# Kernel tuning notes

Hardware: AMD Instinct MI355X
Metric: run time of the kernel (lower is better)

Reference implementation:

```python
import jax, jax.numpy as jnp
import numpy as np

DAYS = 288
DIMS = 40
B, T, N, D = 16, 12, 325, 64
HEAD_DIM = D // 8  # geo(4)+sem(2)+t(2) heads


def setup_inputs() -> dict:
    key = jax.random.key(0)
    ks = jax.random.split(key, 20)
    f = lambda k, s: jax.random.normal(k, s, dtype=jnp.float32)
    inp = {
        "x": f(ks[0], (B, T, N, D)),
        "ind": jax.random.randint(ks[1], (B,), 0, DAYS),
        "x_patterns": jnp.zeros((B, T, N, 1), jnp.float32),
        "pattern_keys": jnp.zeros((B, T, N, 1), jnp.float32),
        "geo_mask": jax.random.randint(ks[2], (N, N), 0, 2).astype(bool),
        # dynamic-graph node embeddings
        "p1": f(ks[3], (DAYS, DIMS)),
        "p2": f(ks[4], (N, DIMS)),
        "p3": f(ks[5], (N, DIMS)),
        "pk": f(ks[6], (DIMS, DIMS, DIMS)),
        # reshape1: Linear(D -> 32)
        "W_r1": f(ks[7], (32, D)) * 0.05, "b_r1": jnp.zeros((32,), jnp.float32),
        # gcn mlp: 1x1 conv, in=(2*1+1)*32=96, out=32
        "W_gcn": f(ks[8], (32, 96)) * 0.05, "b_gcn": jnp.zeros((32,), jnp.float32),
        # reshape2: Linear(32 -> D)
        "W_r2": f(ks[9], (D, 32)) * 0.05, "b_r2": jnp.zeros((D,), jnp.float32),
        # temporal q/k/v 1x1 convs: D -> D*t_ratio = 16, no bias
        "Wtq": f(ks[10], (16, D)) * 0.05,
        "Wtk": f(ks[11], (16, D)) * 0.05,
        "Wtv": f(ks[12], (16, D)) * 0.05,
        # geo q/k/v 1x1 convs: D -> D*geo_ratio = 32, no bias
        "Wgq": f(ks[13], (32, D)) * 0.05,
        "Wgk": f(ks[14], (32, D)) * 0.05,
        "Wgv": f(ks[15], (32, D)) * 0.05,
        # proj: Linear(3D/4 = 48 -> D)
        "W_proj": f(ks[16], (D, 48)) * 0.05, "b_proj": jnp.zeros((D,), jnp.float32),
    }
    return inp


def reference(x, ind, x_patterns, pattern_keys, geo_mask,
              p1, p2, p3, pk,
              W_r1, b_r1, W_gcn, b_gcn, W_r2, b_r2,
              Wtq, Wtk, Wtv, Wgq, Wgk, Wgv, W_proj, b_proj):
    Bx, Tx, Nx, Dx = x.shape
    scale = HEAD_DIM ** -0.5

    # --- dgconstruct: dynamic adjacency [B, N, N]
    te = p1[ind % DAYS]                                  # (B, dims)
    adp = jnp.einsum('ai,ijk->ajk', te, pk)              # (B, dims, dims)
    adp = jnp.einsum('bj,ajk->abk', p2, adp)             # (B, N, dims)
    adp = jnp.einsum('ck,abk->abc', p3, adp)             # (B, N, N)
    adp = jax.nn.softmax(jax.nn.relu(adp), axis=2)

    # --- reshape1 + order-2 GCN + reshape2 (eval mode: dropout off)
    h = jnp.einsum('btnd,cd->bcnt', x, W_r1) + b_r1[None, :, None, None]  # (B,32,N,T)
    x1 = jnp.einsum('ncvl,nwv->ncwl', h, adp)
    x2 = jnp.einsum('ncvl,nwv->ncwl', x1, adp)
    hcat = jnp.concatenate([h, x1, x2], axis=1)          # (B,96,N,T)
    g = jnp.einsum('bcnt,oc->bont', hcat, W_gcn) + b_gcn[None, :, None, None]  # (B,32,N,T)
    xg = jnp.einsum('bont,do->btnd', g, W_r2) + b_r2     # (B,T,N,D)

    # --- temporal attention (2 heads over T, per node)
    t_q = jnp.einsum('btnd,od->bnto', xg, Wtq).reshape(Bx, Nx, Tx, 2, HEAD_DIM).transpose(0, 1, 3, 2, 4)
    t_k = jnp.einsum('btnd,od->bnto', xg, Wtk).reshape(Bx, Nx, Tx, 2, HEAD_DIM).transpose(0, 1, 3, 2, 4)
    t_v = jnp.einsum('btnd,od->bnto', xg, Wtv).reshape(Bx, Nx, Tx, 2, HEAD_DIM).transpose(0, 1, 3, 2, 4)
    t_attn = jax.nn.softmax(jnp.einsum('bnhqd,bnhkd->bnhqk', t_q, t_k) * scale, axis=-1)
    t_x = jnp.einsum('bnhqk,bnhkd->bnhqd', t_attn, t_v)  # (B,N,2,T,hd)
    t_x = t_x.transpose(0, 1, 3, 2, 4).reshape(Bx, Nx, Tx, 2 * HEAD_DIM).transpose(0, 2, 1, 3)  # (B,T,N,16)

    # --- geo attention (4 heads over N, per timestep) with bool mask
    g_q = jnp.einsum('btnd,od->btno', xg, Wgq).reshape(Bx, Tx, Nx, 4, HEAD_DIM).transpose(0, 1, 3, 2, 4)
    g_k = jnp.einsum('btnd,od->btno', xg, Wgk).reshape(Bx, Tx, Nx, 4, HEAD_DIM).transpose(0, 1, 3, 2, 4)
    g_v = jnp.einsum('btnd,od->btno', xg, Wgv).reshape(Bx, Tx, Nx, 4, HEAD_DIM).transpose(0, 1, 3, 2, 4)
    g_attn = jnp.einsum('bthqd,bthkd->bthqk', g_q, g_k) * scale  # (B,T,4,N,N)
    g_attn = jnp.where(geo_mask, -jnp.inf, g_attn)
    g_attn = jax.nn.softmax(g_attn, axis=-1)
    geo_x = jnp.einsum('bthqk,bthkd->bthqd', g_attn, g_v)        # (B,T,4,N,hd)
    geo_x = geo_x.transpose(0, 1, 3, 2, 4).reshape(Bx, Tx, Nx, 4 * HEAD_DIM)  # (B,T,N,32)

    out = jnp.concatenate([t_x, geo_x], axis=-1) @ W_proj.T + b_proj  # (B,T,N,D)
    return out
```

## Files before the change

### kernel.cpp

```cpp
#include <hip/hip_runtime.h>
#include <hip/hip_bf16.h>
#include <math.h>

#define B_ 16
#define T_ 12
#define N_ 325
#define DIMS_ 40
#define DAYS_ 288
#define MW 12
#define NQP 336
#define VP 352

typedef __attribute__((ext_vector_type(8))) short bf16x8;
typedef __attribute__((ext_vector_type(4))) float f32x4;

__device__ __forceinline__ unsigned short cvt1(float f){
  unsigned w;
  asm("v_cvt_pk_bf16_f32 %0, %1, %2" : "=v"(w) : "v"(f), "v"(f));
  return (unsigned short)w;
}
__device__ __forceinline__ unsigned cvt2(float a, float b){
  unsigned w;
  asm("v_cvt_pk_bf16_f32 %0, %1, %2" : "=v"(w) : "v"(a), "v"(b));
  return w;
}
__device__ __forceinline__ bf16x8 u2b(uint4 u){ return __builtin_bit_cast(bf16x8, u); }

__global__ void setup_k(const float* __restrict__ p1, const float* __restrict__ pk,
                        const int* __restrict__ ind, float* __restrict__ A1,
                        const unsigned char* __restrict__ raw, unsigned* __restrict__ bm,
                        const float* __restrict__ p3, float* __restrict__ p3t,
                        const float* W_gcn, const float* b_gcn, const float* W_r2, const float* b_r2,
                        const float* Wtq, const float* Wtk, const float* Wtv,
                        const float* Wgq, const float* Wgk, const float* Wgv,
                        const float* W_proj, const float* W_r1,
                        float* bc, unsigned short* Wcb, unsigned short* Wallb,
                        unsigned short* Wpb, unsigned short* Wr1b){
  int tid = threadIdx.x;
  if (blockIdx.x < 16){
    int b = blockIdx.x;
    __shared__ float te[DIMS_];
    int day = ind[b] % DAYS_; if (day < 0) day += DAYS_;
    for (int i = tid; i < DIMS_; i += blockDim.x) te[i] = p1[day*DIMS_ + i];
    __syncthreads();
    for (int jk = tid; jk < DIMS_*DIMS_; jk += blockDim.x){
      float acc = 0.f;
      for (int i = 0; i < DIMS_; ++i) acc += te[i] * pk[i*DIMS_*DIMS_ + jk];
      A1[b*DIMS_*DIMS_ + jk] = acc;
    }
  } else if (blockIdx.x < 32){
    __shared__ int f1, f3, fo;
    if (tid == 0){ f1 = 0; f3 = 0; fo = 0; }
    __syncthreads();
    for (int i = tid; i < 4096; i += 256){
      unsigned char v = raw[i];
      int m4 = i & 3;
      if (v == 0x3F && m4 == 1) atomicOr(&f1, 1);
      if (v == 0x3F && m4 == 3) atomicOr(&f3, 1);
      if (v != 0 && m4 != 0)    atomicOr(&fo, 1);
    }
    __syncthreads();
    int mode = f1 ? 2 : (f3 ? 3 : (fo ? 0 : 1));
    int idx = (blockIdx.x - 16) * 256 + tid;
    if (idx >= NQP * MW) return;
    int q = idx / MW, w = idx % MW;
    if (q >= N_) { bm[idx] = 0xFFFFFFFFu; return; }
    unsigned bits = 0;
    for (int j = 0; j < 32; ++j){
      int k = w*32 + j;
      int v;
      if (k >= N_) v = 1;
      else {
        size_t i = (size_t)q*N_ + k;
        if (mode == 0)      v = raw[i] != 0;
        else if (mode == 1) v = ((const int*)raw)[i] != 0;
        else if (mode == 2) { unsigned short u = ((const unsigned short*)raw)[i]; v = (u & 0x7FFF) != 0; }
        else                { float f = ((const float*)raw)[i]; v = (f != 0.f); }
      }
      bits |= (unsigned)v << j;
    }
    bm[idx] = bits;
  } else if (blockIdx.x == 32){
    for (int idx = tid; idx < DIMS_*N_; idx += 256){
      int k = idx / N_, c = idx % N_;
      p3t[idx] = p3[c*DIMS_ + k];
    }
  } else if (blockIdx.x == 33){
    __shared__ float WcS[64*96];
    for (int idx = tid; idx < 64*96; idx += 256){
      int d = idx / 96, c = idx % 96;
      float acc = 0.f;
      for (int o = 0; o < 32; ++o) acc += W_r2[d*32 + o] * W_gcn[o*96 + c];
      WcS[idx] = acc;
    }
    for (int d = tid; d < 64; d += 256){
      float acc = b_r2[d];
      for (int o = 0; o < 32; ++o) acc += W_r2[d*32 + o] * b_gcn[o];
      bc[d] = acc;
    }
    __syncthreads();
    for (int idx = tid; idx < 3*4*64*8; idx += 256){
      int jj = idx & 7, rest = idx >> 3;
      int d = rest % 64, gk = rest / 64;
      int g = gk & 3, kc = gk >> 2;
      Wcb[idx] = cvt1(WcS[d*96 + kc*32 + g*8 + jj]);
    }
  } else if (blockIdx.x == 34){
    for (int idx = tid; idx < 2*4*144*8; idx += 256){
      int jj = idx & 7, rest = idx >> 3;
      int j = rest % 144, gk = rest / 144;
      int g = gk & 3, kc = gk >> 2;
      int dd = kc*32 + g*8 + jj;
      const float* src; int rsrc;
      if      (j < 16) { src = Wtq; rsrc = j; }
      else if (j < 32) { src = Wtk; rsrc = j - 16; }
      else if (j < 48) { src = Wtv; rsrc = j - 32; }
      else if (j < 80) { src = Wgq; rsrc = j - 48; }
      else if (j < 112){ src = Wgk; rsrc = j - 80; }
      else             { src = Wgv; rsrc = j - 112; }
      Wallb[idx] = cvt1(src[rsrc*64 + dd]);
    }
  } else if (blockIdx.x == 35){
    for (int idx = tid; idx < 2*4*64*8; idx += 256){
      int jj = idx & 7, rest = idx >> 3;
      int d = rest % 64, gk = rest / 64;
      int g = gk & 3, kc = gk >> 2;
      int k = kc*32 + g*8 + jj;
      Wpb[idx] = (k < 48) ? cvt1(W_proj[d*48 + k]) : (unsigned short)0;
    }
  } else {
    for (int idx = tid; idx < 2*4*32*8; idx += 256){
      int jj = idx & 7, rest = idx >> 3;
      int c = rest % 32, gk = rest / 32;
      int g = gk & 3, kc = gk >> 2;
      Wr1b[idx] = cvt1(W_r1[c*64 + kc*32 + g*8 + jj]);
    }
  }
}

__global__ void dg_adp(const float* __restrict__ p2, const float* __restrict__ p3t,
                       const float* __restrict__ A1, unsigned short* __restrict__ adp_bf){
  int bid = blockIdx.x; int b = bid / N_; int n = bid % N_;
  __shared__ float p2r[DIMS_], t2[DIMS_], sbuf[N_], red[128];
  int tid = threadIdx.x;
  if (tid < DIMS_) p2r[tid] = p2[n*DIMS_ + tid];
  __syncthreads();
  if (tid < DIMS_){
    float acc = 0.f;
    const float* a1 = A1 + b*DIMS_*DIMS_;
    for (int j = 0; j < DIMS_; ++j) acc += p2r[j] * a1[j*DIMS_ + tid];
    t2[tid] = acc;
  }
  __syncthreads();
  float lm = -INFINITY;
  for (int c = tid; c < N_; c += 128){
    float acc = 0.f;
    for (int k = 0; k < DIMS_; ++k) acc += p3t[k*N_ + c] * t2[k];
    acc = fmaxf(acc, 0.f);
    sbuf[c] = acc; lm = fmaxf(lm, acc);
  }
  red[tid] = lm; __syncthreads();
  for (int off = 64; off; off >>= 1){ if (tid < off) red[tid] = fmaxf(red[tid], red[tid+off]); __syncthreads(); }
  float m = red[0]; __syncthreads();
  float ls = 0.f;
  for (int c = tid; c < N_; c += 128){ float e = __expf(sbuf[c] - m); sbuf[c] = e; ls += e; }
  red[tid] = ls; __syncthreads();
  for (int off = 64; off; off >>= 1){ if (tid < off) red[tid] += red[tid+off]; __syncthreads(); }
  float inv = 1.f / red[0];
  unsigned short* outp = adp_bf + ((size_t)b*N_ + n) * VP;
  for (int c = tid; c < VP; c += 128)
    outp[c] = (c < N_) ? cvt1(sbuf[c] * inv) : (unsigned short)0;
}

__global__ __launch_bounds__(256) void hproj_mfma(const float* __restrict__ x,
                                                  const unsigned short* __restrict__ Wr1b,
                                                  const float* __restrict__ b_r1,
                                                  unsigned short* __restrict__ ht,
                                                  unsigned short* __restrict__ hn){
  int tid = threadIdx.x, wv = tid >> 6, ln = tid & 63;
  int bt = blockIdx.x / 6;
  int nt = (blockIdx.x % 6)*4 + wv;
  if (nt >= 21) return;
  int g = ln >> 4, r = ln & 15;
  int n0 = nt*16;
  int nc = min(n0 + r, N_-1);
  int b = bt / T_, t = bt % T_;
  const float* xrow = x + ((size_t)bt*N_ + nc)*64;
  float4 xa = *(const float4*)&xrow[g*8];
  float4 xb = *(const float4*)&xrow[g*8 + 4];
  uint4 u0 = { cvt2(xa.x,xa.y), cvt2(xa.z,xa.w), cvt2(xb.x,xb.y), cvt2(xb.z,xb.w) };
  bf16x8 bv0 = u2b(u0);
  float4 xc = *(const float4*)&xrow[32 + g*8];
  float4 xd = *(const float4*)&xrow[32 + g*8 + 4];
  uint4 u1 = { cvt2(xc.x,xc.y), cvt2(xc.z,xc.w), cvt2(xd.x,xd.y), cvt2(xd.z,xd.w) };
  bf16x8 bv1 = u2b(u1);
  int n = n0 + r;
  #pragma unroll
  for (int ct = 0; ct < 2; ++ct){
    f32x4 acc = {0.f,0.f,0.f,0.f};
    bf16x8 a0 = *(const bf16x8*)&Wr1b[((0*4+g)*32 + ct*16 + r)*8];
    bf16x8 a1 = *(const bf16x8*)&Wr1b[((1*4+g)*32 + ct*16 + r)*8];
    acc = __builtin_amdgcn_mfma_f32_16x16x32_bf16(a0, bv0, acc, 0,0,0);
    acc = __builtin_amdgcn_mfma_f32_16x16x32_bf16(a1, bv1, acc, 0,0,0);
    if (n < N_){
      float v0 = acc[0] + b_r1[ct*16 + g*4 + 0];
      float v1 = acc[1] + b_r1[ct*16 + g*4 + 1];
      float v2 = acc[2] + b_r1[ct*16 + g*4 + 2];
      float v3 = acc[3] + b_r1[ct*16 + g*4 + 3];
      int c0 = ct*16 + g*4;
      ht[((size_t)b*384 + t*32 + c0+0)*VP + n] = cvt1(v0);
      ht[((size_t)b*384 + t*32 + c0+1)*VP + n] = cvt1(v1);
      ht[((size_t)b*384 + t*32 + c0+2)*VP + n] = cvt1(v2);
      ht[((size_t)b*384 + t*32 + c0+3)*VP + n] = cvt1(v3);
      uint2 hp = { cvt2(v0, v1), cvt2(v2, v3) };
      *(uint2*)&hn[((size_t)b*N_ + n)*384 + t*32 + c0] = hp;
    }
  }
}

__global__ __launch_bounds__(256) void gcn_mfma(const unsigned short* __restrict__ adp_bf,
                                                const unsigned short* __restrict__ in_t,
                                                unsigned short* __restrict__ out_t,
                                                unsigned short* __restrict__ out_n){
  int bi = blockIdx.x;
  int b = bi / 36, rest = bi % 36;
  int wt = rest / 6, ctb = rest % 6;
  int tid = threadIdx.x, wv = tid >> 6, ln = tid & 63, g = ln >> 4, r = ln & 15;
  int w0 = wt*64 + wv*16;
  int ct0 = ctb*64;
  int wr = min(w0 + r, N_-1);
  const unsigned short* arow  = adp_bf + ((size_t)b*N_ + wr)*VP;
  const unsigned short* bbase = in_t  + ((size_t)b*384 + ct0)*VP;
  f32x4 acc0={0.f,0.f,0.f,0.f}, acc1=acc0, acc2=acc0, acc3=acc0;
  #pragma unroll
  for (int ks = 0; ks < 11; ++ks){
    int ko = ks*32 + g*8;
    bf16x8 a  = *(const bf16x8*)&arow[ko];
    bf16x8 b0 = *(const bf16x8*)&bbase[(size_t)( 0 + r)*VP + ko];
    bf16x8 b1 = *(const bf16x8*)&bbase[(size_t)(16 + r)*VP + ko];
    bf16x8 b2 = *(const bf16x8*)&bbase[(size_t)(32 + r)*VP + ko];
    bf16x8 b3 = *(const bf16x8*)&bbase[(size_t)(48 + r)*VP + ko];
    acc0 = __builtin_amdgcn_mfma_f32_16x16x32_bf16(a, b0, acc0, 0,0,0);
    acc1 = __builtin_amdgcn_mfma_f32_16x16x32_bf16(a, b1, acc1, 0,0,0);
    acc2 = __builtin_amdgcn_mfma_f32_16x16x32_bf16(a, b2, acc2, 0,0,0);
    acc3 = __builtin_amdgcn_mfma_f32_16x16x32_bf16(a, b3, acc3, 0,0,0);
  }
  f32x4 av[4] = {acc0, acc1, acc2, acc3};
  if (out_t && w0 + 15 < VP){
    #pragma unroll
    for (int dt = 0; dt < 4; ++dt){
      int ct = ct0 + dt*16 + r;
      uint2 pk2 = { cvt2(av[dt][0], av[dt][1]), cvt2(av[dt][2], av[dt][3]) };
      *(uint2*)&out_t[((size_t)b*384 + ct)*VP + w0 + g*4] = pk2;
    }
  }
  #pragma unroll
  for (int dt = 0; dt < 4; ++dt){
    int ct = ct0 + dt*16 + r;
    #pragma unroll
    for (int rg = 0; rg < 4; ++rg){
      int w = w0 + g*4 + rg;
      if (w < N_) out_n[((size_t)b*N_ + w)*384 + ct] = cvt1(av[dt][rg]);
    }
  }
}

__global__ __launch_bounds__(256) void xg_k(const unsigned short* __restrict__ hn,
                                            const unsigned short* __restrict__ x1n,
                                            const unsigned short* __restrict__ x2n,
                                            const unsigned short* __restrict__ Wcb,
                                            const float* __restrict__ bc,
                                            unsigned short* __restrict__ xg_bf){
  int tid = threadIdx.x, wv = tid >> 6, ln = tid & 63;
  int p = blockIdx.x*4 + wv;
  int b = p / N_, n = p % N_;
  int g = ln >> 4, r = ln & 15;
  int rr = min(r, 11);
  size_t base = ((size_t)b*N_ + n)*384;
  bf16x8 a0 = *(const bf16x8*)&hn [base + rr*32 + g*8];
  bf16x8 a1 = *(const bf16x8*)&x1n[base + rr*32 + g*8];
  bf16x8 a2 = *(const bf16x8*)&x2n[base + rr*32 + g*8];
  #pragma unroll
  for (int dt = 0; dt < 4; ++dt){
    f32x4 acc = {0.f,0.f,0.f,0.f};
    bf16x8 b0 = *(const bf16x8*)&Wcb[((0*4+g)*64 + dt*16 + r)*8];
    bf16x8 b1 = *(const bf16x8*)&Wcb[((1*4+g)*64 + dt*16 + r)*8];
    bf16x8 b2 = *(const bf16x8*)&Wcb[((2*4+g)*64 + dt*16 + r)*8];
    acc = __builtin_amdgcn_mfma_f32_16x16x32_bf16(a0, b0, acc, 0,0,0);
    acc = __builtin_amdgcn_mfma_f32_16x16x32_bf16(a1, b1, acc, 0,0,0);
    acc = __builtin_amdgcn_mfma_f32_16x16x32_bf16(a2, b2, acc, 0,0,0);
    float bias = bc[dt*16 + r];
    if (g < 3){
      #pragma unroll
      for (int rg = 0; rg < 4; ++rg){
        int t = g*4 + rg;
        xg_bf[(((size_t)b*T_ + t)*N_ + n)*64 + dt*16 + r] = cvt1(acc[rg] + bias);
      }
    }
  }
}

__global__ __launch_bounds__(256) void qkv_k(const unsigned short* __restrict__ xg_bf,
                                             const unsigned short* __restrict__ Wallb,
                                             float* __restrict__ qkv48,
                                             unsigned short* __restrict__ Qg,
                                             unsigned short* __restrict__ Kg,
                                             unsigned short* __restrict__ Vg){
  int tid = threadIdx.x, wv = tid >> 6, ln = tid & 63;
  int bt = blockIdx.x / 6;
  int nt = (blockIdx.x % 6)*4 + wv;
  if (nt >= 21) return;
  int g = ln >> 4, r = ln & 15;
  int n0 = nt*16;
  int nc = min(n0 + r, N_-1);
  const unsigned short* arow = xg_bf + ((size_t)bt*N_ + nc)*64;
  bf16x8 a0 = *(const bf16x8*)&arow[g*8];
  bf16x8 a1 = *(const bf16x8*)&arow[32 + g*8];
  const float kscale = 0.35355339059327373f * 1.4426950408889634f;
  int hh = r >> 3, dd = r & 7;
  #pragma unroll
  for (int jt = 0; jt < 9; ++jt){
    f32x4 acc = {0.f,0.f,0.f,0.f};
    bf16x8 b0 = *(const bf16x8*)&Wallb[((0*4+g)*144 + jt*16 + r)*8];
    bf16x8 b1 = *(const bf16x8*)&Wallb[((1*4+g)*144 + jt*16 + r)*8];
    acc = __builtin_amdgcn_mfma_f32_16x16x32_bf16(a0, b0, acc, 0,0,0);
    acc = __builtin_amdgcn_mfma_f32_16x16x32_bf16(a1, b1, acc, 0,0,0);
    #pragma unroll
    for (int rg = 0; rg < 4; ++rg){
      int n = n0 + g*4 + rg;
      if (n >= N_) continue;
      float v = acc[rg];
      if (jt < 3){
        qkv48[((size_t)bt*N_ + n)*48 + jt*16 + r] = v;
      } else if (jt < 5){
        int h = (jt-3)*2 + hh;
        Qg[(((size_t)bt*4 + h)*N_ + n)*8 + dd] = cvt1(v);
      } else if (jt < 7){
        int h = (jt-5)*2 + hh;
        Kg[(((size_t)bt*4 + h)*352 + n)*8 + dd] = cvt1(v * kscale);
      } else {
        int h = (jt-7)*2 + hh;
        int m = n & 31, ks = n >> 5;
        int p32 = (((m & 15) >> 2) << 3) | (m & 3) | ((m & 16) >> 2);
        Vg[(((size_t)bt*4 + h)*11 + ks)*512 + dd*32 + p32] = cvt1(v);
      }
    }
  }
}

__global__ __launch_bounds__(256) void attn_fused(const float* __restrict__ qkv48,
                                                  const unsigned short* __restrict__ Qg,
                                                  const unsigned short* __restrict__ Kg,
                                                  const unsigned short* __restrict__ Vg,
                                                  const unsigned* __restrict__ bm,
                                                  float* __restrict__ att){
  __shared__ __align__(16) char smem[17408];
  int bid = blockIdx.x;
  int tid = threadIdx.x, wv = tid >> 6, ln = tid & 63;
  if (bid < 4032){
    unsigned short* Kb = (unsigned short*)smem;
    unsigned short* Vt = (unsigned short*)(smem + 5632);
    int bt = (bid & 7)*24 + (bid >> 3)/21;
    int blkin = (bid >> 3) % 21;
    int unit = blkin*4 + wv;
    int h = unit / 21, tile = unit % 21;
    int g = ln >> 4, r = ln & 15, g4 = g*4;
    bool gzero = (g == 0);
    const bf16x8 z8 = {0,0,0,0,0,0,0,0};
    size_t hb = (size_t)bt*4 + h;
    int qb = tile*16;
    int qc = min(qb + r, N_-1);
    const uint4* bmp = (const uint4*)(bm + (size_t)(qb + r)*MW);
    uint4 m0 = bmp[0], m1 = bmp[1], m2 = bmp[2];
    unsigned bmw[11] = {m0.x,m0.y,m0.z,m0.w, m1.x,m1.y,m1.z,m1.w, m2.x,m2.y,m2.z};
    bf16x8 aq = z8;
    if (gzero) aq = *(const bf16x8*)&Qg[(hb*N_ + qc)*8];
    const unsigned short* Kh = Kg + hb*352*8;
    const unsigned short* Vh = Vg + hb*11*512;
    float ssum = 0.f;
    f32x4 acc = {0.f,0.f,0.f,0.f};
    #pragma unroll
    for (int ks = 0; ks < 11; ++ks){
      bf16x8 akA = z8, akB = z8;
      if (gzero){
        akA = *(const bf16x8*)&Kh[(ks*32 + r)*8];
        akB = *(const bf16x8*)&Kh[(ks*32 + 16 + r)*8];
      }
      f32x4 dA = {0.f,0.f,0.f,0.f}, dB = {0.f,0.f,0.f,0.f};
      dA = __builtin_amdgcn_mfma_f32_16x16x32_bf16(akA, aq, dA, 0,0,0);
      dB = __builtin_amdgcn_mfma_f32_16x16x32_bf16(akB, aq, dB, 0,0,0);
      unsigned wm = bmw[ks];
      unsigned bA = (wm >> g4) & 0xFu;
      unsigned bB = (wm >> (g4 + 16)) & 0xFu;
      float pA[4], pB[4];
      #pragma unroll
      for (int rg = 0; rg < 4; ++rg){
        float eA = exp2f(dA[rg]);
        float eB = exp2f(dB[rg]);
        eA = (bA & (1u << rg)) ? 0.f : eA;
        eB = (bB & (1u << rg)) ? 0.f : eB;
        ssum += eA; ssum += eB;
        pA[rg] = eA; pB[rg] = eB;
      }
      uint4 pw = { cvt2(pA[0],pA[1]), cvt2(pA[2],pA[3]),
                   cvt2(pB[0],pB[1]), cvt2(pB[2],pB[3]) };
      bf16x8 avv = *(const bf16x8*)&Vh[ks*512 + r*32 + g*8];
      acc = __builtin_amdgcn_mfma_f32_16x16x32_bf16(avv, u2b(pw), acc, 0,0,0);
    }
    ssum += __shfl_xor(ssum, 16);
    ssum += __shfl_xor(ssum, 32);
    float inv = (ssum > 0.f) ? __builtin_amdgcn_rcpf(ssum) : 0.f;
    int qq = qb + r;
    if (g < 2 && qq < N_){
      float4 o = make_float4(acc[0]*inv, acc[1]*inv, acc[2]*inv, acc[3]*inv);
      *(float4*)(att + ((size_t)bt*N_ + qq)*48 + 16 + h*8 + g4) = o;
    }
    (void)Kb; (void)Vt;
  } else {
    int p = (bid - 4032)*4 + wv;
    int b = p / N_, n = p % N_;
    float* qs = (float*)smem + (size_t)wv*576;
    float* ss = (float*)(smem + 9216) + (size_t)wv*288;
    for (int idx = ln; idx < T_*48; idx += 64){
      int t = idx / 48, j = idx % 48;
      qs[idx] = qkv48[(((size_t)b*T_ + t)*N_ + n)*48 + j];
    }
    const float scale = 0.35355339059327373f;
    for (int idx = ln; idx < 2*T_*T_; idx += 64){
      int hh = idx / 144, r2 = (idx / T_) % T_, c = idx % T_;
      float acc = 0.f;
      for (int d = 0; d < 8; ++d) acc += qs[r2*48 + hh*8 + d] * qs[c*48 + 16 + hh*8 + d];
      ss[idx] = acc * scale;
    }
    if (ln < 2*T_){
      int hh = ln / T_, r2 = ln % T_;
      float* row = ss + hh*144 + r2*T_;
      float m = -INFINITY; for (int k = 0; k < T_; ++k) m = fmaxf(m, row[k]);
      float s = 0.f; for (int k = 0; k < T_; ++k){ float e = __expf(row[k] - m); row[k] = e; s += e; }
      float inv = 1.f / s; for (int k = 0; k < T_; ++k) row[k] *= inv;
    }
    for (int idx = ln; idx < T_*16; idx += 64){
      int t = idx / 16, o = idx % 16; int hh = o / 8, d = o % 8;
      float acc = 0.f;
      const float* row = ss + hh*144 + t*T_;
      for (int k = 0; k < T_; ++k) acc += row[k] * qs[k*48 + 32 + hh*8 + d];
      att[(((size_t)b*T_ + t)*N_ + n)*48 + o] = acc;
    }
  }
}

__global__ __launch_bounds__(256) void proj_k(const float* __restrict__ att,
                                              const unsigned short* __restrict__ Wpb,
                                              const float* __restrict__ b_proj,
                                              float* __restrict__ out){
  int tid = threadIdx.x, wv = tid >> 6, ln = tid & 63;
  int g = ln >> 4, r = ln & 15;
  long r0 = ((long)blockIdx.x*4 + wv)*16;
  const float* arow = att + (r0 + r)*48;
  float4 qa = *(const float4*)&arow[g*8];
  float4 qb = *(const float4*)&arow[g*8 + 4];
  uint4 u0 = { cvt2(qa.x,qa.y), cvt2(qa.z,qa.w), cvt2(qb.x,qb.y), cvt2(qb.z,qb.w) };
  bf16x8 a0 = u2b(u0);
  bf16x8 a1 = {0,0,0,0,0,0,0,0};
  if (g < 2){
    float4 qc = *(const float4*)&arow[32 + g*8];
    float4 qd = *(const float4*)&arow[36 + g*8];
    uint4 u1 = { cvt2(qc.x,qc.y), cvt2(qc.z,qc.w), cvt2(qd.x,qd.y), cvt2(qd.z,qd.w) };
    a1 = u2b(u1);
  }
  #pragma unroll
  for (int dt = 0; dt < 4; ++dt){
    f32x4 acc = {0.f,0.f,0.f,0.f};
    bf16x8 b0 = *(const bf16x8*)&Wpb[((0*4+g)*64 + dt*16 + r)*8];
    bf16x8 b1 = *(const bf16x8*)&Wpb[((1*4+g)*64 + dt*16 + r)*8];
    acc = __builtin_amdgcn_mfma_f32_16x16x32_bf16(a0, b0, acc, 0,0,0);
    acc = __builtin_amdgcn_mfma_f32_16x16x32_bf16(a1, b1, acc, 0,0,0);
    float bias = b_proj[dt*16 + r];
    #pragma unroll
    for (int rg = 0; rg < 4; ++rg)
      out[(r0 + g*4 + rg)*64 + dt*16 + r] = acc[rg] + bias;
  }
}

extern "C" void kernel_launch(void* const* d_in, const int* in_sizes, int n_in,
                              void* d_out, int out_size, void* d_ws, size_t ws_size,
                              hipStream_t stream){
  const float* x      = (const float*)d_in[0];
  const int*   ind    = (const int*)  d_in[1];
  const unsigned char* gmask_raw = (const unsigned char*)d_in[4];
  const float* p1     = (const float*)d_in[5];
  const float* p2     = (const float*)d_in[6];
  const float* p3     = (const float*)d_in[7];
  const float* pk     = (const float*)d_in[8];
  const float* W_r1   = (const float*)d_in[9];
  const float* b_r1   = (const float*)d_in[10];
  const float* W_gcn  = (const float*)d_in[11];
  const float* b_gcn  = (const float*)d_in[12];
  const float* W_r2   = (const float*)d_in[13];
  const float* b_r2   = (const float*)d_in[14];
  const float* Wtq    = (const float*)d_in[15];
  const float* Wtk    = (const float*)d_in[16];
  const float* Wtv    = (const float*)d_in[17];
  const float* Wgq    = (const float*)d_in[18];
  const float* Wgk    = (const float*)d_in[19];
  const float* Wgv    = (const float*)d_in[20];
  const float* W_proj = (const float*)d_in[21];
  const float* b_proj = (const float*)d_in[22];
  float* out = (float*)d_out;

  float* ws = (float*)d_ws;
  float* A1    = ws; ws += B_*DIMS_*DIMS_;
  float* bc    = ws; ws += 64;
  float* p3t   = ws; ws += DIMS_*N_;
  float* qkv48 = ws; ws += (size_t)B_*T_*N_*48;
  float* att   = ws; ws += (size_t)B_*T_*N_*48;
  unsigned* bm = (unsigned*)ws; ws += NQP*MW;
  unsigned short* us = (unsigned short*)ws;
  unsigned short* adp_bf = us; us += (size_t)B_*N_*VP;
  unsigned short* ht     = us; us += (size_t)B_*384*VP;
  unsigned short* x1t    = us; us += (size_t)B_*384*VP;
  unsigned short* hn     = us; us += (size_t)B_*N_*384;
  unsigned short* x1n    = us; us += (size_t)B_*N_*384;
  unsigned short* x2n    = us; us += (size_t)B_*N_*384;
  unsigned short* xg_bf  = us; us += (size_t)B_*T_*N_*64;
  unsigned short* Qg     = us; us += (size_t)192*4*N_*8;
  unsigned short* Kg     = us; us += (size_t)192*4*352*8;
  unsigned short* Vg     = us; us += (size_t)192*4*11*512;
  unsigned short* Wcb    = us; us += 3*4*64*8;
  unsigned short* Wallb  = us; us += 2*4*144*8;
  unsigned short* Wpb    = us; us += 2*4*64*8;
  unsigned short* Wr1b   = us; us += 2*4*32*8;

  setup_k     <<<37,        256, 0, stream>>>(p1, pk, ind, A1, gmask_raw, bm, p3, p3t,
                                              W_gcn, b_gcn, W_r2, b_r2,
                                              Wtq, Wtk, Wtv, Wgq, Wgk, Wgv,
                                              W_proj, W_r1, bc, Wcb, Wallb, Wpb, Wr1b);
  dg_adp      <<<B_*N_,     128, 0, stream>>>(p2, p3t, A1, adp_bf);
  hproj_mfma  <<<192*6,     256, 0, stream>>>(x, Wr1b, b_r1, ht, hn);
  gcn_mfma    <<<B_*36,     256, 0, stream>>>(adp_bf, ht,  x1t, x1n);
  gcn_mfma    <<<B_*36,     256, 0, stream>>>(adp_bf, x1t, (unsigned short*)nullptr, x2n);
  xg_k        <<<(B_*N_)/4, 256, 0, stream>>>(hn, x1n, x2n, Wcb, bc, xg_bf);
  qkv_k       <<<192*6,     256, 0, stream>>>(xg_bf, Wallb, qkv48, Qg, Kg, Vg);
  attn_fused  <<<4032+1300, 256, 0, stream>>>(qkv48, Qg, Kg, Vg, bm, att);
  proj_k      <<<(B_*T_*N_/16)/4, 256, 0, stream>>>(att, Wpb, b_proj, out);
}
```

Baseline: 154.3 us.

## Merge adjacency softmax and input projection into one heterogeneous launch

```diff
diff --git a/kernel.cpp b/kernel.cpp
--- a/kernel.cpp
+++ b/kernel.cpp
@@ -33,9 +33,9 @@
                         const float* W_gcn, const float* b_gcn, const float* W_r2, const float* b_r2,
                         const float* Wtq, const float* Wtk, const float* Wtv,
                         const float* Wgq, const float* Wgk, const float* Wgv,
-                        const float* W_proj, const float* W_r1,
+                        const float* W_proj,
                         float* bc, unsigned short* Wcb, unsigned short* Wallb,
-                        unsigned short* Wpb, unsigned short* Wr1b){
+                        unsigned short* Wpb){
   int tid = threadIdx.x;
   if (blockIdx.x < 16){
     int b = blockIdx.x;
@@ -120,7 +120,7 @@
       else             { src = Wgv; rsrc = j - 112; }
       Wallb[idx] = cvt1(src[rsrc*64 + dd]);
     }
-  } else if (blockIdx.x == 35){
+  } else {
     for (int idx = tid; idx < 2*4*64*8; idx += 256){
       int jj = idx & 7, rest = idx >> 3;
       int d = rest % 64, gk = rest / 64;
@@ -128,92 +128,106 @@
       int k = kc*32 + g*8 + jj;
       Wpb[idx] = (k < 48) ? cvt1(W_proj[d*48 + k]) : (unsigned short)0;
     }
+  }
+}
+
+__global__ __launch_bounds__(256) void mid_k(const float* __restrict__ x,
+                                             const float* __restrict__ W_r1,
+                                             const float* __restrict__ b_r1,
+                                             unsigned short* __restrict__ ht,
+                                             unsigned short* __restrict__ hn,
+                                             const float* __restrict__ p2,
+                                             const float* __restrict__ p3t,
+                                             const float* __restrict__ A1,
+                                             unsigned short* __restrict__ adp_bf){
+  __shared__ float t2s[4][DIMS_];
+  int tid = threadIdx.x, wv = tid >> 6, ln = tid & 63;
+  int bid = blockIdx.x;
+  if (bid < 1152){
+    int bt = bid / 6;
+    int nt = (bid % 6)*4 + wv;
+    if (nt >= 21) return;
+    int g = ln >> 4, r = ln & 15;
+    int n0 = nt*16;
+    int nc = min(n0 + r, N_-1);
+    int b = bt / T_, t = bt % T_;
+    const float* xrow = x + ((size_t)bt*N_ + nc)*64;
+    float4 xa = *(const float4*)&xrow[g*8];
+    float4 xb = *(const float4*)&xrow[g*8 + 4];
+    uint4 u0 = { cvt2(xa.x,xa.y), cvt2(xa.z,xa.w), cvt2(xb.x,xb.y), cvt2(xb.z,xb.w) };
+    bf16x8 bv0 = u2b(u0);
+    float4 xc = *(const float4*)&xrow[32 + g*8];
+    float4 xd = *(const float4*)&xrow[32 + g*8 + 4];
+    uint4 u1 = { cvt2(xc.x,xc.y), cvt2(xc.z,xc.w), cvt2(xd.x,xd.y), cvt2(xd.z,xd.w) };
+    bf16x8 bv1 = u2b(u1);
+    int n = n0 + r;
+    #pragma unroll
+    for (int ct = 0; ct < 2; ++ct){
+      const float* wrow = W_r1 + (ct*16 + r)*64;
+      float4 wa = *(const float4*)&wrow[g*8];
+      float4 wb = *(const float4*)&wrow[g*8 + 4];
+      uint4 ua = { cvt2(wa.x,wa.y), cvt2(wa.z,wa.w), cvt2(wb.x,wb.y), cvt2(wb.z,wb.w) };
+      bf16x8 a0 = u2b(ua);
+      float4 wc = *(const float4*)&wrow[32 + g*8];
+      float4 wd = *(const float4*)&wrow[32 + g*8 + 4];
+      uint4 ub = { cvt2(wc.x,wc.y), cvt2(wc.z,wc.w), cvt2(wd.x,wd.y), cvt2(wd.z,wd.w) };
+      bf16x8 a1 = u2b(ub);
+      f32x4 acc = {0.f,0.f,0.f,0.f};
+      acc = __builtin_amdgcn_mfma_f32_16x16x32_bf16(a0, bv0, acc, 0,0,0);
+      acc = __builtin_amdgcn_mfma_f32_16x16x32_bf16(a1, bv1, acc, 0,0,0);
+      if (n < N_){
+        float v0 = acc[0] + b_r1[ct*16 + g*4 + 0];
+        float v1 = acc[1] + b_r1[ct*16 + g*4 + 1];
+        float v2 = acc[2] + b_r1[ct*16 + g*4 + 2];
+        float v3 = acc[3] + b_r1[ct*16 + g*4 + 3];
+        int c0 = ct*16 + g*4;
+        ht[((size_t)b*384 + t*32 + c0+0)*VP + n] = cvt1(v0);
+        ht[((size_t)b*384 + t*32 + c0+1)*VP + n] = cvt1(v1);
+        ht[((size_t)b*384 + t*32 + c0+2)*VP + n] = cvt1(v2);
+        ht[((size_t)b*384 + t*32 + c0+3)*VP + n] = cvt1(v3);
+        uint2 hp = { cvt2(v0, v1), cvt2(v2, v3) };
+        *(uint2*)&hn[((size_t)b*N_ + n)*384 + t*32 + c0] = hp;
+      }
+    }
   } else {
-    for (int idx = tid; idx < 2*4*32*8; idx += 256){
-      int jj = idx & 7, rest = idx >> 3;
-      int c = rest % 32, gk = rest / 32;
-      int g = gk & 3, kc = gk >> 2;
-      Wr1b[idx] = cvt1(W_r1[c*64 + kc*32 + g*8 + jj]);
-    }
-  }
-}
-
-__global__ void dg_adp(const float* __restrict__ p2, const float* __restrict__ p3t,
-                       const float* __restrict__ A1, unsigned short* __restrict__ adp_bf){
-  int bid = blockIdx.x; int b = bid / N_; int n = bid % N_;
-  __shared__ float p2r[DIMS_], t2[DIMS_], sbuf[N_], red[128];
-  int tid = threadIdx.x;
-  if (tid < DIMS_) p2r[tid] = p2[n*DIMS_ + tid];
-  __syncthreads();
-  if (tid < DIMS_){
-    float acc = 0.f;
+    int p = (bid - 1152)*4 + wv;
+    int b = p / N_, n = p % N_;
     const float* a1 = A1 + b*DIMS_*DIMS_;
-    for (int j = 0; j < DIMS_; ++j) acc += p2r[j] * a1[j*DIMS_ + tid];
-    t2[tid] = acc;
-  }
-  __syncthreads();
-  float lm = -INFINITY;
-  for (int c = tid; c < N_; c += 128){
-    float acc = 0.f;
-    for (int k = 0; k < DIMS_; ++k) acc += p3t[k*N_ + c] * t2[k];
-    acc = fmaxf(acc, 0.f);
-    sbuf[c] = acc; lm = fmaxf(lm, acc);
-  }
-  red[tid] = lm; __syncthreads();
-  for (int off = 64; off; off >>= 1){ if (tid < off) red[tid] = fmaxf(red[tid], red[tid+off]); __syncthreads(); }
-  float m = red[0]; __syncthreads();
-  float ls = 0.f;
-  for (int c = tid; c < N_; c += 128){ float e = __expf(sbuf[c] - m); sbuf[c] = e; ls += e; }
-  red[tid] = ls; __syncthreads();
-  for (int off = 64; off; off >>= 1){ if (tid < off) red[tid] += red[tid+off]; __syncthreads(); }
-  float inv = 1.f / red[0];
-  unsigned short* outp = adp_bf + ((size_t)b*N_ + n) * VP;
-  for (int c = tid; c < VP; c += 128)
-    outp[c] = (c < N_) ? cvt1(sbuf[c] * inv) : (unsigned short)0;
-}
-
-__global__ __launch_bounds__(256) void hproj_mfma(const float* __restrict__ x,
-                                                  const unsigned short* __restrict__ Wr1b,
-                                                  const float* __restrict__ b_r1,
-                                                  unsigned short* __restrict__ ht,
-                                                  unsigned short* __restrict__ hn){
-  int tid = threadIdx.x, wv = tid >> 6, ln = tid & 63;
-  int bt = blockIdx.x / 6;
-  int nt = (blockIdx.x % 6)*4 + wv;
-  if (nt >= 21) return;
-  int g = ln >> 4, r = ln & 15;
-  int n0 = nt*16;
-  int nc = min(n0 + r, N_-1);
-  int b = bt / T_, t = bt % T_;
-  const float* xrow = x + ((size_t)bt*N_ + nc)*64;
-  float4 xa = *(const float4*)&xrow[g*8];
-  float4 xb = *(const float4*)&xrow[g*8 + 4];
-  uint4 u0 = { cvt2(xa.x,xa.y), cvt2(xa.z,xa.w), cvt2(xb.x,xb.y), cvt2(xb.z,xb.w) };
-  bf16x8 bv0 = u2b(u0);
-  float4 xc = *(const float4*)&xrow[32 + g*8];
-  float4 xd = *(const float4*)&xrow[32 + g*8 + 4];
-  uint4 u1 = { cvt2(xc.x,xc.y), cvt2(xc.z,xc.w), cvt2(xd.x,xd.y), cvt2(xd.z,xd.w) };
-  bf16x8 bv1 = u2b(u1);
-  int n = n0 + r;
-  #pragma unroll
-  for (int ct = 0; ct < 2; ++ct){
-    f32x4 acc = {0.f,0.f,0.f,0.f};
-    bf16x8 a0 = *(const bf16x8*)&Wr1b[((0*4+g)*32 + ct*16 + r)*8];
-    bf16x8 a1 = *(const bf16x8*)&Wr1b[((1*4+g)*32 + ct*16 + r)*8];
-    acc = __builtin_amdgcn_mfma_f32_16x16x32_bf16(a0, bv0, acc, 0,0,0);
-    acc = __builtin_amdgcn_mfma_f32_16x16x32_bf16(a1, bv1, acc, 0,0,0);
-    if (n < N_){
-      float v0 = acc[0] + b_r1[ct*16 + g*4 + 0];
-      float v1 = acc[1] + b_r1[ct*16 + g*4 + 1];
-      float v2 = acc[2] + b_r1[ct*16 + g*4 + 2];
-      float v3 = acc[3] + b_r1[ct*16 + g*4 + 3];
-      int c0 = ct*16 + g*4;
-      ht[((size_t)b*384 + t*32 + c0+0)*VP + n] = cvt1(v0);
-      ht[((size_t)b*384 + t*32 + c0+1)*VP + n] = cvt1(v1);
-      ht[((size_t)b*384 + t*32 + c0+2)*VP + n] = cvt1(v2);
-      ht[((size_t)b*384 + t*32 + c0+3)*VP + n] = cvt1(v3);
-      uint2 hp = { cvt2(v0, v1), cvt2(v2, v3) };
-      *(uint2*)&hn[((size_t)b*N_ + n)*384 + t*32 + c0] = hp;
+    const float* p2r = p2 + n*DIMS_;
+    if (ln < DIMS_){
+      float acc = 0.f;
+      for (int jj = 0; jj < DIMS_; ++jj) acc += p2r[jj] * a1[jj*DIMS_ + ln];
+      t2s[wv][ln] = acc;
+    }
+    float sc[6];
+    float lm = -1e30f;
+    #pragma unroll
+    for (int i = 0; i < 6; ++i){
+      int c = ln + i*64;
+      float acc = 0.f;
+      if (c < N_){
+        for (int k = 0; k < DIMS_; ++k) acc += p3t[k*N_ + c] * t2s[wv][k];
+        acc = fmaxf(acc, 0.f);
+        lm = fmaxf(lm, acc);
+      }
+      sc[i] = acc;
+    }
+    #pragma unroll
+    for (int off = 32; off; off >>= 1) lm = fmaxf(lm, __shfl_xor(lm, off));
+    float ls = 0.f;
+    #pragma unroll
+    for (int i = 0; i < 6; ++i){
+      int c = ln + i*64;
+      if (c < N_){ float e = __expf(sc[i] - lm); sc[i] = e; ls += e; }
+    }
+    #pragma unroll
+    for (int off = 32; off; off >>= 1) ls += __shfl_xor(ls, off);
+    float inv = 1.f / ls;
+    unsigned short* outp = adp_bf + ((size_t)b*N_ + n) * VP;
+    #pragma unroll
+    for (int i = 0; i < 6; ++i){
+      int c = ln + i*64;
+      if (c < VP) outp[c] = (c < N_) ? cvt1(sc[i] * inv) : (unsigned short)0;
     }
   }
 }
@@ -358,8 +372,6 @@
   int bid = blockIdx.x;
   int tid = threadIdx.x, wv = tid >> 6, ln = tid & 63;
   if (bid < 4032){
-    unsigned short* Kb = (unsigned short*)smem;
-    unsigned short* Vt = (unsigned short*)(smem + 5632);
     int bt = (bid & 7)*24 + (bid >> 3)/21;
     int blkin = (bid >> 3) % 21;
     int unit = blkin*4 + wv;
@@ -415,7 +427,6 @@
       float4 o = make_float4(acc[0]*inv, acc[1]*inv, acc[2]*inv, acc[3]*inv);
       *(float4*)(att + ((size_t)bt*N_ + qq)*48 + 16 + h*8 + g4) = o;
     }
-    (void)Kb; (void)Vt;
   } else {
     int p = (bid - 4032)*4 + wv;
     int b = p / N_, n = p % N_;
@@ -529,14 +540,12 @@
   unsigned short* Wcb    = us; us += 3*4*64*8;
   unsigned short* Wallb  = us; us += 2*4*144*8;
   unsigned short* Wpb    = us; us += 2*4*64*8;
-  unsigned short* Wr1b   = us; us += 2*4*32*8;
-
-  setup_k     <<<37,        256, 0, stream>>>(p1, pk, ind, A1, gmask_raw, bm, p3, p3t,
+
+  setup_k     <<<36,        256, 0, stream>>>(p1, pk, ind, A1, gmask_raw, bm, p3, p3t,
                                               W_gcn, b_gcn, W_r2, b_r2,
                                               Wtq, Wtk, Wtv, Wgq, Wgk, Wgv,
-                                              W_proj, W_r1, bc, Wcb, Wallb, Wpb, Wr1b);
-  dg_adp      <<<B_*N_,     128, 0, stream>>>(p2, p3t, A1, adp_bf);
-  hproj_mfma  <<<192*6,     256, 0, stream>>>(x, Wr1b, b_r1, ht, hn);
+                                              W_proj, bc, Wcb, Wallb, Wpb);
+  mid_k       <<<1152+1300, 256, 0, stream>>>(x, W_r1, b_r1, ht, hn, p2, p3t, A1, adp_bf);
   gcn_mfma    <<<B_*36,     256, 0, stream>>>(adp_bf, ht,  x1t, x1n);
   gcn_mfma    <<<B_*36,     256, 0, stream>>>(adp_bf, x1t, (unsigned short*)nullptr, x2n);
   xg_k        <<<(B_*N_)/4, 256, 0, stream>>>(hn, x1n, x2n, Wcb, bc, xg_bf);
```

New measurement: 182.2 us. 18.0% more time.
